# Kernel optimization log

Hardware: AMD Instinct MI355X
Metric: run time of the kernel (lower is better)

Reference implementation:

```python
import jax, jax.numpy as jnp
import numpy as np

EMBED = 1024
HEADS = 16
HEAD_DIM = EMBED // HEADS
T = 1024
B = 2
TEMP = 1.0
EPS = 1e-20


def setup_inputs() -> dict:
    key = jax.random.key(0)
    ks = jax.random.split(key, 8)
    s = 0.02  # xavier-ish init scale
    return {
        "g": jax.random.normal(ks[0], (T, B, EMBED), dtype=jnp.float32),
        "h": jax.random.normal(ks[1], (T, B, EMBED), dtype=jnp.float32),
        "g_in_w": jax.random.normal(ks[2], (3 * EMBED, EMBED), dtype=jnp.float32) * s,
        "g_in_b": jnp.zeros((3 * EMBED,), dtype=jnp.float32),
        "h_in_w": jax.random.normal(ks[3], (2 * EMBED, EMBED), dtype=jnp.float32) * s,
        "h_in_b": jnp.zeros((2 * EMBED,), dtype=jnp.float32),
        "g_out_w": jax.random.normal(ks[4], (EMBED, EMBED), dtype=jnp.float32) * s,
        "g_out_b": jnp.zeros((EMBED,), dtype=jnp.float32),
        "h_out_w": jax.random.normal(ks[5], (EMBED, EMBED), dtype=jnp.float32) * s,
        "h_out_b": jnp.zeros((EMBED,), dtype=jnp.float32),
    }


def reference(g, h, g_in_w, g_in_b, h_in_w, h_in_b, g_out_w, g_out_b, h_out_w, h_out_b):
    Tt, Bb, E = g.shape
    H, d = HEADS, HEAD_DIM

    # fused qkv projection on g stream, kv on h stream (F.linear: x @ W^T + b)
    q, gk, gv = jnp.split(g @ g_in_w.T + g_in_b, 3, axis=-1)
    hk, hv = jnp.split(h @ h_in_w.T + h_in_b, 2, axis=-1)
    q = q * (d ** -0.5)

    def to_heads(x):  # [T,B,E] -> [B,H,T,d]
        return x.reshape(Tt, Bb, H, d).transpose(1, 2, 0, 3)

    q, gk, gv, hk, hv = map(to_heads, (q, gk, gv, hk, hv))

    # dual-stream attention scores
    g_scores = jnp.einsum("bhtd,bhsd->bhts", q, gk)
    h_scores = jnp.einsum("bhtd,bhsd->bhts", q, hk)

    g_p = jax.nn.softmax(g_scores, axis=-1)
    h_p = jax.nn.softmax(h_scores, axis=-1)

    # gumbel-softmax sample of h_scores (mode='gumbel', temperature=TEMP)
    u = jax.random.uniform(jax.random.key(42), h_scores.shape, dtype=h_scores.dtype)
    noise = -jnp.log(-jnp.log(u + EPS) + EPS)
    sample = jax.nn.softmax((jax.nn.log_softmax(h_scores, axis=-1) + noise) / TEMP, axis=-1)

    g_attn = jnp.einsum("bhts,bhsd->bhtd", g_p, gv)
    h_attn = jnp.einsum("bhts,bhsd->bhtd", sample, hv)

    def merge(x):  # [B,H,T,d] -> [T,B,E]
        return x.transpose(2, 0, 1, 3).reshape(Tt, Bb, E)

    g_out = merge(g_attn) @ g_out_w.T + g_out_b
    h_out = merge(h_attn) @ h_out_w.T + h_out_b
    return g_out, h_out
```

## Files before the change

### kernel.cpp

```cpp
#include <hip/hip_runtime.h>
#include <stdint.h>

#define T_SEQ 1024

typedef __attribute__((ext_vector_type(8))) short short8;
typedef __attribute__((ext_vector_type(4))) float f32x4;
typedef __attribute__((ext_vector_type(4))) unsigned short ushort4v;
typedef __attribute__((ext_vector_type(8))) unsigned short ushort8v;

__device__ __forceinline__ unsigned short f2bf(float f) {
  union { float f; uint32_t u; } v; v.f = f;
  return (unsigned short)((v.u + 0x7fffu + ((v.u >> 16) & 1u)) >> 16);
}
__device__ __forceinline__ float bf2f(unsigned short u) {
  union { uint32_t u; float f; } v; v.u = ((uint32_t)u) << 16;
  return v.f;
}

__device__ __forceinline__ uint32_t tf_bits(uint32_t flat) {
  const uint32_t ks1 = 42u;
  const uint32_t ks2 = 0x1BD11BDAu ^ 42u;
  uint32_t x0 = 0u;
  uint32_t x1 = flat + ks1;
#define TFR(r) { x0 += x1; x1 = (x1 << (r)) | (x1 >> (32 - (r))); x1 ^= x0; }
  TFR(13) TFR(15) TFR(26) TFR(6)
  x0 += ks1; x1 += ks2 + 1u;
  TFR(17) TFR(29) TFR(16) TFR(24)
  x0 += ks2; x1 += 2u;
  TFR(13) TFR(15) TFR(26) TFR(6)
  x1 += ks1 + 3u;
  TFR(17) TFR(29) TFR(16) TFR(24)
  x0 += ks1; x1 += ks2 + 4u;
  TFR(13) TFR(15) TFR(26) TFR(6)
  x0 += ks2; x1 += 5u;
#undef TFR
  return x0 ^ x1;
}

__device__ __forceinline__ float gumbel_noise(uint32_t flat) {
  const uint32_t bits = tf_bits(flat);
  const float u = __uint_as_float((bits >> 9) | 0x3f800000u) - 1.0f;
  return -__logf(-__logf(u + 1e-20f) + 1e-20f);
}

__global__ __launch_bounds__(256) void convert_pre(
    const float* __restrict__ g, const float* __restrict__ h,
    const float* __restrict__ wgi_f, const float* __restrict__ whi_f,
    const float* __restrict__ wgo_f, const float* __restrict__ who_f,
    unsigned short* __restrict__ gbf, unsigned short* __restrict__ hbf,
    unsigned short* __restrict__ wgi, unsigned short* __restrict__ whi,
    unsigned short* __restrict__ wgo, unsigned short* __restrict__ who)
{
  const int64_t Q_SPLIT = 1048576;
  const int64_t Q_TOTAL = Q_SPLIT + 1835008;
  for (int64_t qd = (int64_t)blockIdx.x * 256 + threadIdx.x; qd < Q_TOTAL;
       qd += (int64_t)gridDim.x * 256) {
    if (qd < Q_SPLIT) {
      const int which = qd >= 524288;
      const int64_t e = (qd - (which ? 524288 : 0)) * 4;
      const float4 v = *(const float4*)((which ? h : g) + e);
      ushort4v u = {f2bf(v.x), f2bf(v.y), f2bf(v.z), f2bf(v.w)};
      *(ushort4v*)((which ? hbf : gbf) + e) = u;
    } else {
      int64_t off = qd - Q_SPLIT;
      const float* src; unsigned short* dst;
      if (off < 786432)                 { src = wgi_f; dst = wgi; }
      else if (off < 1310720)           { off -= 786432;  src = whi_f; dst = whi; }
      else if (off < 1572864)           { off -= 1310720; src = wgo_f; dst = wgo; }
      else                              { off -= 1572864; src = who_f; dst = who; }
      const int64_t e = off * 4;
      const float4 v = *(const float4*)(src + e);
      ushort4v u = {f2bf(v.x), f2bf(v.y), f2bf(v.z), f2bf(v.w)};
      *(ushort4v*)(dst + e) = u;
    }
  }
}

template<int TM, bool BF16OUT>
__device__ __forceinline__ void gemm_plain_core(
    const unsigned short* __restrict__ Ab, const unsigned short* __restrict__ Wb,
    const float* __restrict__ bias, int N, int K, int m0, int n0,
    int scale_limit, void* Cout, unsigned short* sA, unsigned short* sW)
{
  const int tid = threadIdx.x;
  const int w = tid >> 6;
  const int lane = tid & 63;
  const int txl = lane & 15, q = lane >> 4;
  const int wr = (w >> 1) * (TM * 16);
  const int wc = (w & 1) << 6;
  const int TPR = 8 / TM;
  const int arow = tid / TPR;
  const int acol = (tid % TPR) * (8 * TM);
  const int wrow = tid >> 1;
  const int wcol = (tid & 1) << 5;

  f32x4 acc[TM][4];
#pragma unroll
  for (int i = 0; i < TM; i++)
#pragma unroll
    for (int j = 0; j < 4; j++) acc[i][j] = (f32x4){0.f, 0.f, 0.f, 0.f};

  for (int k0 = 0; k0 < K; k0 += 64) {
    const unsigned short* Ap = Ab + (size_t)(m0 + arow) * K + k0 + acol;
    const unsigned short* Wp = Wb + (size_t)(n0 + wrow) * K + k0 + wcol;
    ushort8v a8[TM], w8[4];
#pragma unroll
    for (int e = 0; e < TM; e++) a8[e] = *(const ushort8v*)(Ap + 8 * e);
#pragma unroll
    for (int e = 0; e < 4; e++)  w8[e] = *(const ushort8v*)(Wp + 8 * e);
    __syncthreads();
#pragma unroll
    for (int e = 0; e < TM; e++) *(ushort8v*)&sA[arow * 72 + acol + 8 * e] = a8[e];
#pragma unroll
    for (int e = 0; e < 4; e++)  *(ushort8v*)&sW[wrow * 72 + wcol + 8 * e] = w8[e];
    __syncthreads();
#pragma unroll
    for (int kk = 0; kk < 2; kk++) {
      short8 af[TM], wf[4];
#pragma unroll
      for (int i = 0; i < TM; i++)
        af[i] = *(const short8*)&sA[(wr + 16 * i + txl) * 72 + 32 * kk + 8 * q];
#pragma unroll
      for (int j = 0; j < 4; j++)
        wf[j] = *(const short8*)&sW[(wc + 16 * j + txl) * 72 + 32 * kk + 8 * q];
#pragma unroll
      for (int i = 0; i < TM; i++)
#pragma unroll
        for (int j = 0; j < 4; j++)
          acc[i][j] = __builtin_amdgcn_mfma_f32_16x16x32_bf16(af[i], wf[j], acc[i][j], 0, 0, 0);
    }
  }

#pragma unroll
  for (int j = 0; j < 4; j++) {
    const int col = n0 + wc + 16 * j + txl;
    const float bj = bias[col];
    const float sc = (col < scale_limit) ? 0.125f : 1.0f;
#pragma unroll
    for (int i = 0; i < TM; i++) {
      const int rbase = m0 + wr + 16 * i + 4 * q;
#pragma unroll
      for (int r = 0; r < 4; r++) {
        const float v = (acc[i][j][r] + bj) * sc;
        if (BF16OUT) ((unsigned short*)Cout)[(size_t)(rbase + r) * N + col] = f2bf(v);
        else         ((float*)Cout)[(size_t)(rbase + r) * N + col] = v;
      }
    }
  }
}

__global__ __launch_bounds__(256, 4) void gemm_inproj(
    const unsigned short* __restrict__ gbf, const unsigned short* __restrict__ wgi,
    const float* __restrict__ bgi,
    const unsigned short* __restrict__ hbf, const unsigned short* __restrict__ whi,
    const float* __restrict__ bhi,
    unsigned short* __restrict__ qkv, unsigned short* __restrict__ hkv)
{
  __shared__ __align__(16) unsigned short sm[18432];
  const int bx = blockIdx.x;
  const int m0 = blockIdx.y * 128;
  if (bx < 24)
    gemm_plain_core<4, true>(gbf, wgi, bgi, 3072, 1024, m0, bx * 128, 1024,
                             qkv, sm, sm + 9216);
  else
    gemm_plain_core<4, true>(hbf, whi, bhi, 2048, 1024, m0, (bx - 24) * 128, 0,
                             hkv, sm, sm + 9216);
}

__global__ __launch_bounds__(256, 2) void gemm_outproj(
    const unsigned short* __restrict__ attnb,
    const unsigned short* __restrict__ wgo, const float* __restrict__ bgo,
    const unsigned short* __restrict__ who, const float* __restrict__ bho,
    float* __restrict__ out)
{
  __shared__ __align__(16) unsigned short sm[13824];
  const int m0 = blockIdx.y * 64;
  const unsigned short* Wp = (m0 < 2048) ? wgo : who;
  const float* bp = (m0 < 2048) ? bgo : bho;
  gemm_plain_core<2, false>(attnb, Wp, bp, 1024, 1024, m0, blockIdx.x * 128, 0,
                            out, sm, sm + 4608);
}

__global__ __launch_bounds__(256, 4) void attn_mfma(
    const unsigned short* __restrict__ qkv, const unsigned short* __restrict__ hkv,
    float* __restrict__ Opart, float* __restrict__ lpart)
{
  __shared__ __align__(16) unsigned short smem[18432];
  unsigned short* KV = smem;
  unsigned short* PC = smem + 9216;
  unsigned short* QS = smem + 9216;

  const int tid = threadIdx.x;
  const int w = tid >> 6;
  const int lane = tid & 63;
  const int txl = lane & 15, q = lane >> 4;
  const int t0 = blockIdx.x * 64;
  const int bh = blockIdx.y;
  const int z = blockIdx.z;
  const int b = bh >> 4;
  const int head = bh & 15;
  const int hoff = head * 64;
  const int sr = tid >> 2;
  const int sc = (tid & 3) << 4;

  {
    const size_t gq = ((size_t)(t0 + sr) * 2 + b) * 3072 + hoff + sc;
    *(ushort8v*)&QS[sr * 72 + sc]     = *(const ushort8v*)&qkv[gq];
    *(ushort8v*)&QS[sr * 72 + sc + 8] = *(const ushort8v*)&qkv[gq + 8];
  }
  __syncthreads();
  const short8 aq0 = *(const short8*)&QS[(16 * w + txl) * 72 + 8 * q];
  const short8 aq1 = *(const short8*)&QS[(16 * w + txl) * 72 + 32 + 8 * q];

  f32x4 Og[4], Oh[4];
  float l_g[4], l_h[4];
#pragma unroll
  for (int i = 0; i < 4; i++) {
    Og[i] = (f32x4){0.f, 0.f, 0.f, 0.f};
    Oh[i] = (f32x4){0.f, 0.f, 0.f, 0.f};
    l_g[i] = 0.f; l_h[i] = 0.f;
  }

  unsigned short* pcg = PC + (w * 2 + 0) * 1152;
  unsigned short* pch = PC + (w * 2 + 1) * 1152;

  const int s_begin = z * (T_SEQ / 2);
  const int s_end = s_begin + (T_SEQ / 2);
  for (int s0 = s_begin; s0 < s_end; s0 += 64) {
    __syncthreads();
    {
      const size_t grow = (size_t)(s0 + sr) * 2 + b;
      const ushort8v kg0 = *(const ushort8v*)&qkv[grow * 3072 + 1024 + hoff + sc];
      const ushort8v kg1 = *(const ushort8v*)&qkv[grow * 3072 + 1024 + hoff + sc + 8];
      const ushort8v kh0 = *(const ushort8v*)&hkv[grow * 2048 + hoff + sc];
      const ushort8v kh1 = *(const ushort8v*)&hkv[grow * 2048 + hoff + sc + 8];
      *(ushort8v*)&KV[sr * 72 + sc]            = kg0;
      *(ushort8v*)&KV[sr * 72 + sc + 8]        = kg1;
      *(ushort8v*)&KV[4608 + sr * 72 + sc]     = kh0;
      *(ushort8v*)&KV[4608 + sr * 72 + sc + 8] = kh1;
    }
    __syncthreads();

    f32x4 Sg[4], Sh[4];
    const f32x4 zz = (f32x4){0.f, 0.f, 0.f, 0.f};
#pragma unroll
    for (int nt = 0; nt < 4; nt++) {
      const int srw = (16 * nt + txl) * 72;
      const short8 bg0 = *(const short8*)&KV[srw + 8 * q];
      const short8 bg1 = *(const short8*)&KV[srw + 32 + 8 * q];
      const short8 bh0 = *(const short8*)&KV[4608 + srw + 8 * q];
      const short8 bh1 = *(const short8*)&KV[4608 + srw + 32 + 8 * q];
      f32x4 ag = __builtin_amdgcn_mfma_f32_16x16x32_bf16(aq0, bg0, zz, 0, 0, 0);
      ag = __builtin_amdgcn_mfma_f32_16x16x32_bf16(aq1, bg1, ag, 0, 0, 0);
      f32x4 ah = __builtin_amdgcn_mfma_f32_16x16x32_bf16(aq0, bh0, zz, 0, 0, 0);
      ah = __builtin_amdgcn_mfma_f32_16x16x32_bf16(aq1, bh1, ah, 0, 0, 0);
      Sg[nt] = ag; Sh[nt] = ah;
    }

#pragma unroll
    for (int nt = 0; nt < 4; nt++)
#pragma unroll
      for (int r = 0; r < 4; r++) {
        const uint32_t trow = (uint32_t)(t0 + 16 * w + 4 * q + r);
        const uint32_t scol_ = (uint32_t)(s0 + 16 * nt + txl);
        Sh[nt][r] += gumbel_noise(((uint32_t)bh << 20) | (trow << 10) | scol_);
      }

#pragma unroll
    for (int nt = 0; nt < 4; nt++) {
      float eg[4], eh[4];
#pragma unroll
      for (int r = 0; r < 4; r++) {
        eg[r] = __expf(Sg[nt][r]); l_g[r] += eg[r];
        eh[r] = __expf(Sh[nt][r]); l_h[r] += eh[r];
      }
      const int sbase = (16 * nt + txl) * 18 + 4 * q;
      *(uint32_t*)&pcg[sbase]     = (uint32_t)f2bf(eg[0]) | ((uint32_t)f2bf(eg[1]) << 16);
      *(uint32_t*)&pcg[sbase + 2] = (uint32_t)f2bf(eg[2]) | ((uint32_t)f2bf(eg[3]) << 16);
      *(uint32_t*)&pch[sbase]     = (uint32_t)f2bf(eh[0]) | ((uint32_t)f2bf(eh[1]) << 16);
      *(uint32_t*)&pch[sbase + 2] = (uint32_t)f2bf(eh[2]) | ((uint32_t)f2bf(eh[3]) << 16);
    }

    __syncthreads();
    {
      const int dd = tid >> 2;
      const int sseg = (tid & 3) * 16;
      ushort8v vg[2], vh[2];
#pragma unroll
      for (int p = 0; p < 2; p++)
#pragma unroll
        for (int m = 0; m < 8; m++) {
          const int s = sseg + 8 * p + m;
          const size_t grow = (size_t)(s0 + s) * 2 + b;
          vg[p][m] = qkv[grow * 3072 + 2048 + hoff + dd];
          vh[p][m] = hkv[grow * 2048 + 1024 + hoff + dd];
        }
#pragma unroll
      for (int p = 0; p < 2; p++) {
        *(ushort8v*)&KV[dd * 72 + sseg + 8 * p]        = vg[p];
        *(ushort8v*)&KV[4608 + dd * 72 + sseg + 8 * p] = vh[p];
      }
    }
    __syncthreads();

#pragma unroll
    for (int c = 0; c < 2; c++) {
      short8 apg, aph;
#pragma unroll
      for (int j = 0; j < 8; j++) {
        apg[j] = (short)pcg[(32 * c + 8 * q + j) * 18 + txl];
        aph[j] = (short)pch[(32 * c + 8 * q + j) * 18 + txl];
      }
#pragma unroll
      for (int nt = 0; nt < 4; nt++) {
        const int drow = (16 * nt + txl) * 72;
        const short8 bvg = *(const short8*)&KV[drow + 32 * c + 8 * q];
        const short8 bvh = *(const short8*)&KV[4608 + drow + 32 * c + 8 * q];
        Og[nt] = __builtin_amdgcn_mfma_f32_16x16x32_bf16(apg, bvg, Og[nt], 0, 0, 0);
        Oh[nt] = __builtin_amdgcn_mfma_f32_16x16x32_bf16(aph, bvh, Oh[nt], 0, 0, 0);
      }
    }
  }

  float* opg = Opart + ((size_t)(z * 2 + 0) * 2048) * 1024;
  float* oph = Opart + ((size_t)(z * 2 + 1) * 2048) * 1024;
  float* lpg = lpart + (size_t)(z * 2 + 0) * 2048 * 16;
  float* lph = lpart + (size_t)(z * 2 + 1) * 2048 * 16;
#pragma unroll
  for (int r = 0; r < 4; r++) {
    float lg = l_g[r], lh = l_h[r];
    lg += __shfl_xor(lg, 1); lg += __shfl_xor(lg, 2);
    lg += __shfl_xor(lg, 4); lg += __shfl_xor(lg, 8);
    lh += __shfl_xor(lh, 1); lh += __shfl_xor(lh, 2);
    lh += __shfl_xor(lh, 4); lh += __shfl_xor(lh, 8);
    const int row = (t0 + 16 * w + 4 * q + r) * 2 + b;
    if (txl == 0) {
      lpg[row * 16 + head] = lg;
      lph[row * 16 + head] = lh;
    }
    const size_t base = (size_t)row * 1024 + hoff;
#pragma unroll
    for (int nt = 0; nt < 4; nt++) {
      opg[base + 16 * nt + txl] = Og[nt][r];
      oph[base + 16 * nt + txl] = Oh[nt][r];
    }
  }
}

__global__ __launch_bounds__(256) void merge_attn(
    const float* __restrict__ Opart, const float* __restrict__ lpart,
    unsigned short* __restrict__ attnb)
{
  const int idx = blockIdx.x * 256 + threadIdx.x;
  const int st = idx >> 19;
  const int i = idx & 0x7FFFF;
  const int row = i >> 8;
  const int colq = i & 255;
  const int head = colq >> 4;
  const float4 o0 = *(const float4*)&Opart[((size_t)(0 + st) * 2048 + row) * 1024 + colq * 4];
  const float4 o1 = *(const float4*)&Opart[((size_t)(2 + st) * 2048 + row) * 1024 + colq * 4];
  const float l0 = lpart[(size_t)(0 + st) * 32768 + row * 16 + head];
  const float l1 = lpart[(size_t)(2 + st) * 32768 + row * 16 + head];
  const float inv = 1.0f / (l0 + l1);
  ushort4v u = {f2bf((o0.x + o1.x) * inv), f2bf((o0.y + o1.y) * inv),
                f2bf((o0.z + o1.z) * inv), f2bf((o0.w + o1.w) * inv)};
  *(ushort4v*)&attnb[((size_t)st * 2048 + row) * 1024 + colq * 4] = u;
}

extern "C" void kernel_launch(void* const* d_in, const int* in_sizes, int n_in,
                              void* d_out, int out_size, void* d_ws, size_t ws_size,
                              hipStream_t stream) {
  const float* g       = (const float*)d_in[0];
  const float* h       = (const float*)d_in[1];
  const float* g_in_w  = (const float*)d_in[2];
  const float* g_in_b  = (const float*)d_in[3];
  const float* h_in_w  = (const float*)d_in[4];
  const float* h_in_b  = (const float*)d_in[5];
  const float* g_out_w = (const float*)d_in[6];
  const float* g_out_b = (const float*)d_in[7];
  const float* h_out_w = (const float*)d_in[8];
  const float* h_out_b = (const float*)d_in[9];
  float* out = (float*)d_out;

  unsigned short* ws = (unsigned short*)d_ws;
  unsigned short* qkv   = ws;
  unsigned short* hkv   = qkv + (size_t)2048*3072;
  unsigned short* attnb = hkv + (size_t)2048*2048;
  unsigned short* wgo   = attnb + (size_t)4096*1024;
  unsigned short* who   = wgo + (size_t)1024*1024;
  unsigned short* scratch = who + (size_t)1024*1024;
  unsigned short* gbf = scratch;
  unsigned short* hbf = gbf + (size_t)2048*1024;
  unsigned short* wgi = hbf + (size_t)2048*1024;
  unsigned short* whi = wgi + (size_t)3072*1024;
  float* Opart = (float*)scratch;
  float* lpart = Opart + (size_t)4*2048*1024;

  convert_pre<<<1024, 256, 0, stream>>>(g, h, g_in_w, h_in_w, g_out_w, h_out_w,
                                        gbf, hbf, wgi, whi, wgo, who);
  gemm_inproj<<<dim3(40, 16), 256, 0, stream>>>(
      gbf, wgi, g_in_b, hbf, whi, h_in_b, qkv, hkv);
  attn_mfma<<<dim3(T_SEQ / 64, 32, 2), 256, 0, stream>>>(qkv, hkv, Opart, lpart);
  merge_attn<<<4096, 256, 0, stream>>>(Opart, lpart, attnb);
  gemm_outproj<<<dim3(8, 64), 256, 0, stream>>>(
      attnb, wgo, g_out_b, who, h_out_b, out);
}
```

Measured before the change: 285.2 us.

## Load GEMM tiles directly to LDS with XOR-swizzled layout

Replaces the register-staged global→LDS copy in the shared GEMM core with direct global_load_lds 16-byte transfers. It also switches the padded 72-stride LDS layout to a 64-stride XOR-swizzled one, which shrinks shared memory. The aim is to cut VGPR use and the extra LDS write instructions in the in- and out-projection GEMMs. It still uses two barriers per k-step and adds no prefetch overlap, and it relies on the swizzle being correct for the direct-load lane mapping.

New measurement: 282.4 us. No clear change (-1.0%).

```diff
diff --git a/kernel.cpp b/kernel.cpp
--- a/kernel.cpp
+++ b/kernel.cpp
@@ -15,6 +15,12 @@
 __device__ __forceinline__ float bf2f(unsigned short u) {
   union { uint32_t u; float f; } v; v.u = ((uint32_t)u) << 16;
   return v.f;
+}
+
+__device__ __forceinline__ void gl2lds16(const unsigned short* g, unsigned short* l) {
+  __builtin_amdgcn_global_load_lds(
+      (const __attribute__((address_space(1))) void*)g,
+      (__attribute__((address_space(3))) void*)l, 16, 0, 0);
 }
 
 __device__ __forceinline__ uint32_t tf_bits(uint32_t flat) {
@@ -88,11 +94,13 @@
   const int txl = lane & 15, q = lane >> 4;
   const int wr = (w >> 1) * (TM * 16);
   const int wc = (w & 1) << 6;
-  const int TPR = 8 / TM;
-  const int arow = tid / TPR;
-  const int acol = (tid % TPR) * (8 * TM);
-  const int wrow = tid >> 1;
-  const int wcol = (tid & 1) << 5;
+  const int lr = lane >> 3, lu = lane & 7;
+  const int rx7 = txl & 7;
+
+  const unsigned short* Asrc = Ab + (size_t)(m0 + w * 8 * TM + lr) * K + ((lu ^ lr) << 3);
+  const unsigned short* Wsrc = Wb + (size_t)(n0 + w * 32 + lr) * K + ((lu ^ lr) << 3);
+  unsigned short* sAd = sA + (w * 8 * TM) * 64;
+  unsigned short* sWd = sW + (w * 32) * 64;
 
   f32x4 acc[TM][4];
 #pragma unroll
@@ -101,28 +109,24 @@
     for (int j = 0; j < 4; j++) acc[i][j] = (f32x4){0.f, 0.f, 0.f, 0.f};
 
   for (int k0 = 0; k0 < K; k0 += 64) {
-    const unsigned short* Ap = Ab + (size_t)(m0 + arow) * K + k0 + acol;
-    const unsigned short* Wp = Wb + (size_t)(n0 + wrow) * K + k0 + wcol;
-    ushort8v a8[TM], w8[4];
-#pragma unroll
-    for (int e = 0; e < TM; e++) a8[e] = *(const ushort8v*)(Ap + 8 * e);
-#pragma unroll
-    for (int e = 0; e < 4; e++)  w8[e] = *(const ushort8v*)(Wp + 8 * e);
-    __syncthreads();
-#pragma unroll
-    for (int e = 0; e < TM; e++) *(ushort8v*)&sA[arow * 72 + acol + 8 * e] = a8[e];
-#pragma unroll
-    for (int e = 0; e < 4; e++)  *(ushort8v*)&sW[wrow * 72 + wcol + 8 * e] = w8[e];
+    __syncthreads();
+#pragma unroll
+    for (int i = 0; i < TM; i++)
+      gl2lds16(Asrc + (size_t)(8 * i) * K + k0, sAd + (8 * i) * 64);
+#pragma unroll
+    for (int i = 0; i < 4; i++)
+      gl2lds16(Wsrc + (size_t)(8 * i) * K + k0, sWd + (8 * i) * 64);
     __syncthreads();
 #pragma unroll
     for (int kk = 0; kk < 2; kk++) {
+      const int uoff = ((4 * kk + q) ^ rx7) << 3;
       short8 af[TM], wf[4];
 #pragma unroll
       for (int i = 0; i < TM; i++)
-        af[i] = *(const short8*)&sA[(wr + 16 * i + txl) * 72 + 32 * kk + 8 * q];
+        af[i] = *(const short8*)&sA[(wr + 16 * i + txl) * 64 + uoff];
 #pragma unroll
       for (int j = 0; j < 4; j++)
-        wf[j] = *(const short8*)&sW[(wc + 16 * j + txl) * 72 + 32 * kk + 8 * q];
+        wf[j] = *(const short8*)&sW[(wc + 16 * j + txl) * 64 + uoff];
 #pragma unroll
       for (int i = 0; i < TM; i++)
 #pragma unroll
@@ -156,15 +160,15 @@
     const float* __restrict__ bhi,
     unsigned short* __restrict__ qkv, unsigned short* __restrict__ hkv)
 {
-  __shared__ __align__(16) unsigned short sm[18432];
+  __shared__ __align__(16) unsigned short sm[16384];
   const int bx = blockIdx.x;
   const int m0 = blockIdx.y * 128;
   if (bx < 24)
     gemm_plain_core<4, true>(gbf, wgi, bgi, 3072, 1024, m0, bx * 128, 1024,
-                             qkv, sm, sm + 9216);
+                             qkv, sm, sm + 8192);
   else
     gemm_plain_core<4, true>(hbf, whi, bhi, 2048, 1024, m0, (bx - 24) * 128, 0,
-                             hkv, sm, sm + 9216);
+                             hkv, sm, sm + 8192);
 }
 
 __global__ __launch_bounds__(256, 2) void gemm_outproj(
@@ -173,12 +177,12 @@
     const unsigned short* __restrict__ who, const float* __restrict__ bho,
     float* __restrict__ out)
 {
-  __shared__ __align__(16) unsigned short sm[13824];
+  __shared__ __align__(16) unsigned short sm[12288];
   const int m0 = blockIdx.y * 64;
   const unsigned short* Wp = (m0 < 2048) ? wgo : who;
   const float* bp = (m0 < 2048) ? bgo : bho;
   gemm_plain_core<2, false>(attnb, Wp, bp, 1024, 1024, m0, blockIdx.x * 128, 0,
-                            out, sm, sm + 4608);
+                            out, sm, sm + 4096);
 }
 
 __global__ __launch_bounds__(256, 4) void attn_mfma(
```
